# Kernel optimization log

Measured on AMD Instinct MI355X. Metric: run time of the kernel, lower is better.

Reference implementation:

```python
import jax, jax.numpy as jnp
import numpy as np

N_NODES = 100000
N_EDGES = 600000
DIMS = [128, 64, 32, 2]


def gcn_conv(x, edge_index, W, b, n_nodes):
    """PyG GCNConv (eval mode): symmetric-normalized aggregation with self-loops.
    out = D^{-1/2} (A + I) D^{-1/2} (x W) + b
    """
    h = x @ W  # [N, out] -- transform first (cheaper when out < in)
    src = jnp.concatenate([edge_index[0], jnp.arange(n_nodes)])  # add self-loops
    dst = jnp.concatenate([edge_index[1], jnp.arange(n_nodes)])
    deg = jax.ops.segment_sum(jnp.ones_like(dst, dtype=h.dtype), dst,
                              num_segments=n_nodes)  # in-degree incl. self-loop
    dinv = jax.lax.rsqrt(deg)
    norm = dinv[src] * dinv[dst]  # [E+N]
    msg = norm[:, None] * h[src]  # gather + scale
    out = jax.ops.segment_sum(msg, dst, num_segments=n_nodes)  # scatter-add
    return out + b


def setup_inputs() -> dict:
    key = jax.random.key(0)
    ks = jax.random.split(key, 8)
    x = jax.random.normal(ks[0], (N_NODES, DIMS[0]), dtype=jnp.float32)
    edge_index = jax.random.randint(ks[1], (2, N_EDGES), 0, N_NODES, dtype=jnp.int64)
    inp = {"x": x, "edge_index": edge_index}
    for i in range(3):
        fan_in, fan_out = DIMS[i], DIMS[i + 1]
        s = 1.0 / np.sqrt(fan_in)
        inp[f"W{i+1}"] = jax.random.uniform(ks[2 + 2 * i], (fan_in, fan_out),
                                            minval=-s, maxval=s, dtype=jnp.float32)
        inp[f"b{i+1}"] = jnp.zeros((fan_out,), dtype=jnp.float32)
    return inp


def reference(x, edge_index, W1, b1, W2, b2, W3, b3):
    # 3 stacked GCNConv layers with ReLU; dropout is identity in eval mode.
    n = x.shape[0]
    x = jax.nn.relu(gcn_conv(x, edge_index, W1, b1, n))
    x = jax.nn.relu(gcn_conv(x, edge_index, W2, b2, n))
    x = jax.nn.relu(gcn_conv(x, edge_index, W3, b3, n))
    return x
```

## Files before the change

### kernel.cpp

```cpp
#include <hip/hip_runtime.h>
#include <math.h>


#define FULL_GRID 2048
#define PARTS 8

typedef const __attribute__((address_space(1))) void* gas_ptr;
typedef __attribute__((address_space(3))) void* las_ptr;

__device__ __forceinline__ void gld16(const void* g, void* l) {
  __builtin_amdgcn_global_load_lds((gas_ptr)g, (las_ptr)l, 16, 0, 0);
}

__global__ __launch_bounds__(256) void k_zero(int* __restrict__ p, int n4) {
  int i = blockIdx.x * blockDim.x + threadIdx.x;
  const int stride = gridDim.x * blockDim.x;
  int4* p4 = (int4*)p;
  for (; i < n4; i += stride) p4[i] = make_int4(0, 0, 0, 0);
}

__global__ __launch_bounds__(256) void k_detect(const unsigned int* __restrict__ words,
                                                int* __restrict__ flag) {
  __shared__ int sm[256];
  int cnt = 0;
  #pragma unroll
  for (int j = 0; j < 8; ++j) {
    int idx = (threadIdx.x * 8 + j) * 2 + 1;
    cnt += (words[idx] == 0u) ? 1 : 0;
  }
  sm[threadIdx.x] = cnt;
  __syncthreads();
  for (int off = 128; off > 0; off >>= 1) {
    if (threadIdx.x < off) sm[threadIdx.x] += sm[threadIdx.x + off];
    __syncthreads();
  }
  if (threadIdx.x == 0) flag[0] = (sm[0] > 1024) ? 1 : 0;
}

__global__ __launch_bounds__(256) void k_hist(const void* __restrict__ eraw, int E,
                                              int N, const int* __restrict__ flag,
                                              int* __restrict__ counts) {
  const int is64 = flag[0];
  const int part = blockIdx.x & (PARTS - 1);
  const int lo = (int)((long long)N * part / PARTS);
  const int hi = (int)((long long)N * (part + 1) / PARTS);
  int i = (blockIdx.x >> 3) * blockDim.x + threadIdx.x;
  const int stride = (gridDim.x >> 3) * blockDim.x;
  if (is64) {
    const long long* e = (const long long*)eraw;
    for (; i < E; i += stride) {
      const int d = (int)e[(long long)E + i];
      if (d >= lo && d < hi) atomicAdd(&counts[d], 1);
    }
  } else {
    const int* e = (const int*)eraw;
    for (; i < E; i += stride) {
      const int d = e[E + i];
      if (d >= lo && d < hi) atomicAdd(&counts[d], 1);
    }
  }
}

__global__ __launch_bounds__(1024) void k_scan1(const int* __restrict__ counts,
                                                int* __restrict__ scanned,
                                                int* __restrict__ partials, int n) {
  __shared__ int sm[1024];
  const int i = blockIdx.x * 1024 + threadIdx.x;
  const int v = (i < n) ? counts[i] : 0;
  sm[threadIdx.x] = v;
  __syncthreads();
  for (int off = 1; off < 1024; off <<= 1) {
    int t = sm[threadIdx.x];
    int u = (threadIdx.x >= off) ? sm[threadIdx.x - off] : 0;
    __syncthreads();
    sm[threadIdx.x] = t + u;
    __syncthreads();
  }
  const int inc = sm[threadIdx.x];
  if (i < n) scanned[i] = inc - v;
  if (threadIdx.x == 1023) partials[blockIdx.x] = inc;
}

__global__ __launch_bounds__(1024) void k_scan2(int* __restrict__ partials, int nb) {
  __shared__ int sm[1024];
  const int v = (threadIdx.x < nb) ? partials[threadIdx.x] : 0;
  sm[threadIdx.x] = v;
  __syncthreads();
  for (int off = 1; off < 1024; off <<= 1) {
    int t = sm[threadIdx.x];
    int u = (threadIdx.x >= off) ? sm[threadIdx.x - off] : 0;
    __syncthreads();
    sm[threadIdx.x] = t + u;
    __syncthreads();
  }
  if (threadIdx.x < nb) partials[threadIdx.x] = sm[threadIdx.x] - v;
}

__global__ __launch_bounds__(256) void k_scan3(const int* __restrict__ scanned,
                                               const int* __restrict__ partials,
                                               const int* __restrict__ counts,
                                               int* __restrict__ offsets,
                                               int* __restrict__ cursor,
                                               float* __restrict__ dinv, int n) {
  int i = blockIdx.x * blockDim.x + threadIdx.x;
  const int stride = gridDim.x * blockDim.x;
  for (; i < n; i += stride) {
    const int o = scanned[i] + partials[i >> 10];
    offsets[i] = o;
    cursor[i] = o;
    dinv[i] = rsqrtf((float)counts[i] + 1.0f);
  }
}

__global__ __launch_bounds__(256) void k_fill(const void* __restrict__ eraw, int E,
                                              int N, const int* __restrict__ flag,
                                              int* __restrict__ cursor,
                                              int* __restrict__ elist) {
  const int is64 = flag[0];
  const int part = blockIdx.x & (PARTS - 1);
  const int lo = (int)((long long)N * part / PARTS);
  const int hi = (int)((long long)N * (part + 1) / PARTS);
  int i = (blockIdx.x >> 3) * blockDim.x + threadIdx.x;
  const int stride = (gridDim.x >> 3) * blockDim.x;
  if (is64) {
    const long long* e = (const long long*)eraw;
    for (; i < E; i += stride) {
      const int d = (int)e[(long long)E + i];
      if (d >= lo && d < hi) {
        const int s = (int)e[i];
        elist[atomicAdd(&cursor[d], 1)] = s;
      }
    }
  } else {
    const int* e = (const int*)eraw;
    for (; i < E; i += stride) {
      const int d = e[E + i];
      if (d >= lo && d < hi) {
        const int s = e[i];
        elist[atomicAdd(&cursor[d], 1)] = s;
      }
    }
  }
}

template <int F_IN, int F_OUT, int TILE_M, int KC, int THREADS>
__global__ __launch_bounds__(THREADS) void k_transform(const float* __restrict__ X,
                                                       const float* __restrict__ W,
                                                       const float* __restrict__ dinv,
                                                       float* __restrict__ H, int n) {
  constexpr int COLT = F_OUT / 4;
  constexpr int ROWT = THREADS / COLT;
  constexpr int TM = TILE_M / ROWT;
  constexpr int NKC = F_IN / KC;
  constexpr int K4 = F_IN / 4;
  constexpr int NWB = (NKC > 1) ? 2 : 1;
  static_assert(TM * ROWT == TILE_M && COLT * 4 == F_OUT, "tiling");
  static_assert((TILE_M * F_IN * 4) % 1024 == 0 && (KC * F_OUT * 4) % 1024 == 0, "segs");
  static_assert(K4 >= 8, "swizzle range");
  static_assert(ROWT % 8 == 0, "swizzle invariance across r");

  __shared__ __align__(16) float Xs[TILE_M * F_IN];
  __shared__ __align__(16) float Ws[NWB][KC * F_OUT];

  const int tid = threadIdx.x;
  const int lane = tid & 63;
  const int wid = tid >> 6;
  constexpr int NWAVES = THREADS / 64;
  const long long base = (long long)blockIdx.x * TILE_M;

  const float4* __restrict__ X4 = (const float4*)X;
  if (base + TILE_M <= n) {
    constexpr int SEGS = TILE_M * F_IN * 4 / 1024;
    constexpr int PW = SEGS / NWAVES;
    #pragma unroll
    for (int j = 0; j < PW; ++j) {
      const int seg = wid * PW + j;
      const int slot = seg * 64 + lane;
      const int row = slot / K4;
      const int c = slot % K4;
      const int ksrc = c ^ (row & 7);
      gld16(&X4[(base + row) * K4 + ksrc], &Xs[seg * 256]);
    }
  } else {
    for (int slot = tid; slot < TILE_M * K4; slot += THREADS) {
      const int row = slot / K4;
      const int c = slot % K4;
      float4 v = make_float4(0.f, 0.f, 0.f, 0.f);
      if (base + row < n) v = X4[(base + row) * K4 + (c ^ (row & 7))];
      ((float4*)Xs)[slot] = v;
    }
  }

  constexpr int WSEG = KC * F_OUT * 4 / 1024;
  constexpr int WPW = WSEG / NWAVES;
  static_assert(WPW >= 1, "W seg per wave");
  {
    #pragma unroll
    for (int j = 0; j < WPW; ++j) {
      const int seg = wid * WPW + j;
      gld16(W + seg * 256 + lane * 4, &Ws[0][seg * 256]);
    }
  }

  const int ct = tid % COLT;
  const int rt = tid / COLT;
  const int sw = rt & 7;

  float4 acc[TM];
  #pragma unroll
  for (int r = 0; r < TM; ++r) acc[r] = make_float4(0.f, 0.f, 0.f, 0.f);

  const float4* Xs4 = (const float4*)Xs;

  for (int kc = 0; kc < NKC; ++kc) {
    __syncthreads();
    if (NKC > 1 && kc + 1 < NKC) {
      const float* wb = W + (kc + 1) * KC * F_OUT;
      #pragma unroll
      for (int j = 0; j < WPW; ++j) {
        const int seg = wid * WPW + j;
        gld16(wb + seg * 256 + lane * 4, &Ws[(kc + 1) & (NWB - 1)][seg * 256]);
      }
    }
    const float4* Ws4 = (const float4*)Ws[kc & (NWB - 1)];
    #pragma unroll
    for (int k4 = 0; k4 < KC / 4; ++k4) {
      const int kk = kc * (KC / 4) + k4;
      float4 wv0 = Ws4[(k4 * 4 + 0) * COLT + ct];
      float4 wv1 = Ws4[(k4 * 4 + 1) * COLT + ct];
      float4 wv2 = Ws4[(k4 * 4 + 2) * COLT + ct];
      float4 wv3 = Ws4[(k4 * 4 + 3) * COLT + ct];
      #pragma unroll
      for (int r = 0; r < TM; ++r) {
        const float4 xv = Xs4[(rt + r * ROWT) * K4 + (kk ^ sw)];
        acc[r].x = fmaf(xv.x, wv0.x, acc[r].x);
        acc[r].y = fmaf(xv.x, wv0.y, acc[r].y);
        acc[r].z = fmaf(xv.x, wv0.z, acc[r].z);
        acc[r].w = fmaf(xv.x, wv0.w, acc[r].w);
        acc[r].x = fmaf(xv.y, wv1.x, acc[r].x);
        acc[r].y = fmaf(xv.y, wv1.y, acc[r].y);
        acc[r].z = fmaf(xv.y, wv1.z, acc[r].z);
        acc[r].w = fmaf(xv.y, wv1.w, acc[r].w);
        acc[r].x = fmaf(xv.z, wv2.x, acc[r].x);
        acc[r].y = fmaf(xv.z, wv2.y, acc[r].y);
        acc[r].z = fmaf(xv.z, wv2.z, acc[r].z);
        acc[r].w = fmaf(xv.z, wv2.w, acc[r].w);
        acc[r].x = fmaf(xv.w, wv3.x, acc[r].x);
        acc[r].y = fmaf(xv.w, wv3.y, acc[r].y);
        acc[r].z = fmaf(xv.w, wv3.z, acc[r].z);
        acc[r].w = fmaf(xv.w, wv3.w, acc[r].w);
      }
    }
  }

  #pragma unroll
  for (int r = 0; r < TM; ++r) {
    const long long row = base + rt + r * ROWT;
    if (row < n) {
      const float di = dinv[row];
      float4 v = acc[r];
      v.x *= di; v.y *= di; v.z *= di; v.w *= di;
      *(float4*)&H[row * F_OUT + ct * 4] = v;
    }
  }
}

template <int F, bool RELU_OUT, bool FUSE_W3>
__global__ __launch_bounds__(256) void k_aggregate(const float* __restrict__ HS,
                                                   const float* __restrict__ dinv,
                                                   const int* __restrict__ offsets,
                                                   const int* __restrict__ counts,
                                                   const int* __restrict__ elist,
                                                   const float* __restrict__ bias,
                                                   const float* __restrict__ W3,
                                                   float* __restrict__ out, int n) {
  const int f = threadIdx.x % F;
  const int grp = threadIdx.x / F;
  constexpr int GRPS = 256 / F;
  const float bf = bias[f];
  float w30 = 0.f, w31 = 0.f;
  if (FUSE_W3) { w30 = W3[f * 2 + 0]; w31 = W3[f * 2 + 1]; }

  for (long long d = (long long)blockIdx.x * GRPS + grp; d < n;
       d += (long long)gridDim.x * GRPS) {
    const float di = dinv[d];
    float acc = HS[d * F + f];
    const int start = offsets[d];
    const int cnt = counts[d];
    for (int j = 0; j < cnt; j += 8) {
      int idx[8];
      float v[8];
      #pragma unroll
      for (int t = 0; t < 8; ++t) {
        const int jj = (j + t < cnt) ? (j + t) : j;
        idx[t] = elist[start + jj];
      }
      #pragma unroll
      for (int t = 0; t < 8; ++t) v[t] = HS[(long long)idx[t] * F + f];
      #pragma unroll
      for (int t = 0; t < 8; ++t) acc += (j + t < cnt) ? v[t] : 0.f;
    }

    float r = fmaf(di, acc, bf);
    if (RELU_OUT) r = fmaxf(r, 0.f);
    if (!FUSE_W3) {
      out[d * F + f] = r;
    } else {
      float t0 = r * w30, t1 = r * w31;
      #pragma unroll
      for (int m = 1; m < 32; m <<= 1) {
        t0 += __shfl_xor(t0, m, 64);
        t1 += __shfl_xor(t1, m, 64);
      }
      if (f == 0) {
        out[d * 2 + 0] = di * t0;
        out[d * 2 + 1] = di * t1;
      }
    }
  }
}

extern "C" void kernel_launch(void* const* d_in, const int* in_sizes, int n_in,
                              void* d_out, int out_size, void* d_ws, size_t ws_size,
                              hipStream_t stream) {
  const float* x = (const float*)d_in[0];
  const void* eraw = d_in[1];
  const float* W1 = (const float*)d_in[2];
  const float* b1 = (const float*)d_in[3];
  const float* W2 = (const float*)d_in[4];
  const float* b2 = (const float*)d_in[5];
  const float* W3 = (const float*)d_in[6];
  const float* b3 = (const float*)d_in[7];
  float* out = (float*)d_out;

  const int N = in_sizes[0] / 128;
  const int E = in_sizes[1] / 2;

  char* ws = (char*)d_ws;
  size_t off = 0;
  auto alloc = [&](size_t bytes) -> char* {
    char* p = ws + off;
    off = (off + bytes + 255) & ~(size_t)255;
    return p;
  };
  int*   flag     = (int*)alloc(256);
  int*   counts   = (int*)alloc((size_t)N * 4 + 16);
  int*   scanned  = (int*)alloc((size_t)N * 4);
  int*   partials = (int*)alloc(1024 * 4);
  int*   offsets  = (int*)alloc((size_t)N * 4);
  int*   cursor   = (int*)alloc((size_t)N * 4);
  int*   elist    = (int*)alloc((size_t)E * 4);
  float* dinv     = (float*)alloc((size_t)N * 4);
  float* hbuf     = (float*)alloc((size_t)N * 64 * 4);
  float* obuf     = (float*)alloc((size_t)N * 64 * 4);
  float* h2buf    = (float*)alloc((size_t)N * 32 * 4);
  (void)ws_size; (void)n_in; (void)out_size;

  k_zero<<<128, 256, 0, stream>>>(counts, (N + 3) / 4);
  k_detect<<<1, 256, 0, stream>>>((const unsigned int*)eraw, flag);
  k_hist<<<FULL_GRID, 256, 0, stream>>>(eraw, E, N, flag, counts);
  const int NB = (N + 1023) >> 10;
  k_scan1<<<NB, 1024, 0, stream>>>(counts, scanned, partials, N);
  k_scan2<<<1, 1024, 0, stream>>>(partials, NB);
  k_scan3<<<(N + 255) / 256, 256, 0, stream>>>(scanned, partials, counts, offsets,
                                               cursor, dinv, N);
  k_fill<<<FULL_GRID, 256, 0, stream>>>(eraw, E, N, flag, cursor, elist);

  k_transform<128, 64, 128, 16, 256><<<(N + 127) / 128, 256, 0, stream>>>(
      x, W1, dinv, hbuf, N);
  k_aggregate<64, true, false><<<(N + 3) / 4, 256, 0, stream>>>(
      hbuf, dinv, offsets, counts, elist, b1, nullptr, obuf, N);

  k_transform<64, 32, 128, 64, 256><<<(N + 127) / 128, 256, 0, stream>>>(
      obuf, W2, dinv, h2buf, N);
  k_aggregate<32, true, true><<<(N + 7) / 8, 256, 0, stream>>>(
      h2buf, dinv, offsets, counts, elist, b2, W3, hbuf, N);

  k_aggregate<2, true, false><<<(N + 127) / 128, 256, 0, stream>>>(
      hbuf, dinv, offsets, counts, elist, b3, nullptr, out, N);
}
```

Measured before the change: 197.1 us.

## Make transform kernel persistent with resident W and double-buffered X tiles

After: 190.7 us. -3.2%, faster.

```diff
diff --git a/kernel.cpp b/kernel.cpp
--- a/kernel.cpp
+++ b/kernel.cpp
@@ -143,96 +143,91 @@
   }
 }
 
-template <int F_IN, int F_OUT, int TILE_M, int KC, int THREADS>
+template <int F_IN, int F_OUT, int TILE_M, int THREADS>
 __global__ __launch_bounds__(THREADS) void k_transform(const float* __restrict__ X,
                                                        const float* __restrict__ W,
                                                        const float* __restrict__ dinv,
-                                                       float* __restrict__ H, int n) {
+                                                       float* __restrict__ H, int n,
+                                                       int ntiles) {
   constexpr int COLT = F_OUT / 4;
   constexpr int ROWT = THREADS / COLT;
   constexpr int TM = TILE_M / ROWT;
-  constexpr int NKC = F_IN / KC;
   constexpr int K4 = F_IN / 4;
-  constexpr int NWB = (NKC > 1) ? 2 : 1;
+  constexpr int NWAVES = THREADS / 64;
+  constexpr int XSEG = TILE_M * F_IN * 4 / 1024;
+  constexpr int XPW = XSEG / NWAVES;
+  constexpr int WSEG = F_IN * F_OUT * 4 / 1024;
+  constexpr int WPW = (WSEG + NWAVES - 1) / NWAVES;
   static_assert(TM * ROWT == TILE_M && COLT * 4 == F_OUT, "tiling");
-  static_assert((TILE_M * F_IN * 4) % 1024 == 0 && (KC * F_OUT * 4) % 1024 == 0, "segs");
+  static_assert(XPW * NWAVES == XSEG, "X segs per wave");
   static_assert(K4 >= 8, "swizzle range");
   static_assert(ROWT % 8 == 0, "swizzle invariance across r");
 
-  __shared__ __align__(16) float Xs[TILE_M * F_IN];
-  __shared__ __align__(16) float Ws[NWB][KC * F_OUT];
+  __shared__ __align__(16) float Xs[2][TILE_M * F_IN];
+  __shared__ __align__(16) float Ws[F_IN * F_OUT];
 
   const int tid = threadIdx.x;
   const int lane = tid & 63;
   const int wid = tid >> 6;
-  constexpr int NWAVES = THREADS / 64;
-  const long long base = (long long)blockIdx.x * TILE_M;
-
   const float4* __restrict__ X4 = (const float4*)X;
-  if (base + TILE_M <= n) {
-    constexpr int SEGS = TILE_M * F_IN * 4 / 1024;
-    constexpr int PW = SEGS / NWAVES;
-    #pragma unroll
-    for (int j = 0; j < PW; ++j) {
-      const int seg = wid * PW + j;
-      const int slot = seg * 64 + lane;
-      const int row = slot / K4;
-      const int c = slot % K4;
-      const int ksrc = c ^ (row & 7);
-      gld16(&X4[(base + row) * K4 + ksrc], &Xs[seg * 256]);
-    }
-  } else {
-    for (int slot = tid; slot < TILE_M * K4; slot += THREADS) {
-      const int row = slot / K4;
-      const int c = slot % K4;
-      float4 v = make_float4(0.f, 0.f, 0.f, 0.f);
-      if (base + row < n) v = X4[(base + row) * K4 + (c ^ (row & 7))];
-      ((float4*)Xs)[slot] = v;
-    }
-  }
-
-  constexpr int WSEG = KC * F_OUT * 4 / 1024;
-  constexpr int WPW = WSEG / NWAVES;
-  static_assert(WPW >= 1, "W seg per wave");
-  {
-    #pragma unroll
-    for (int j = 0; j < WPW; ++j) {
-      const int seg = wid * WPW + j;
-      gld16(W + seg * 256 + lane * 4, &Ws[0][seg * 256]);
-    }
-  }
+
+  #pragma unroll
+  for (int j = 0; j < WPW; ++j) {
+    const int seg = wid * WPW + j;
+    if (seg < WSEG) gld16(W + seg * 256 + lane * 4, &Ws[seg * 256]);
+  }
+
+  auto stage = [&](int buf, int tile) {
+    const long long base = (long long)tile * TILE_M;
+    if (base + TILE_M <= n) {
+      #pragma unroll
+      for (int j = 0; j < XPW; ++j) {
+        const int seg = wid * XPW + j;
+        const int slot = seg * 64 + lane;
+        const int row = slot / K4;
+        const int c = slot % K4;
+        gld16(&X4[(base + row) * K4 + (c ^ (row & 7))], &Xs[buf][seg * 256]);
+      }
+    } else {
+      for (int slot = tid; slot < TILE_M * K4; slot += THREADS) {
+        const int row = slot / K4;
+        const int c = slot % K4;
+        float4 v = make_float4(0.f, 0.f, 0.f, 0.f);
+        if (base + row < n) v = X4[(base + row) * K4 + (c ^ (row & 7))];
+        ((float4*)Xs[buf])[slot] = v;
+      }
+    }
+  };
 
   const int ct = tid % COLT;
   const int rt = tid / COLT;
   const int sw = rt & 7;
-
-  float4 acc[TM];
-  #pragma unroll
-  for (int r = 0; r < TM; ++r) acc[r] = make_float4(0.f, 0.f, 0.f, 0.f);
-
-  const float4* Xs4 = (const float4*)Xs;
-
-  for (int kc = 0; kc < NKC; ++kc) {
-    __syncthreads();
-    if (NKC > 1 && kc + 1 < NKC) {
-      const float* wb = W + (kc + 1) * KC * F_OUT;
-      #pragma unroll
-      for (int j = 0; j < WPW; ++j) {
-        const int seg = wid * WPW + j;
-        gld16(wb + seg * 256 + lane * 4, &Ws[(kc + 1) & (NWB - 1)][seg * 256]);
-      }
-    }
-    const float4* Ws4 = (const float4*)Ws[kc & (NWB - 1)];
+  const float4* Ws4 = (const float4*)Ws;
+
+  int tile = blockIdx.x;
+  if (tile < ntiles) stage(0, tile);
+  int buf = 0;
+
+  for (; tile < ntiles; tile += gridDim.x) {
+    __syncthreads();
+    const int nxt = tile + gridDim.x;
+    if (nxt < ntiles) stage(buf ^ 1, nxt);
+
+    const long long base = (long long)tile * TILE_M;
+    float4 acc[TM];
     #pragma unroll
-    for (int k4 = 0; k4 < KC / 4; ++k4) {
-      const int kk = kc * (KC / 4) + k4;
-      float4 wv0 = Ws4[(k4 * 4 + 0) * COLT + ct];
-      float4 wv1 = Ws4[(k4 * 4 + 1) * COLT + ct];
-      float4 wv2 = Ws4[(k4 * 4 + 2) * COLT + ct];
-      float4 wv3 = Ws4[(k4 * 4 + 3) * COLT + ct];
+    for (int r = 0; r < TM; ++r) acc[r] = make_float4(0.f, 0.f, 0.f, 0.f);
+    const float4* Xs4 = (const float4*)Xs[buf];
+
+    #pragma unroll 4
+    for (int k4 = 0; k4 < K4; ++k4) {
+      const float4 wv0 = Ws4[(k4 * 4 + 0) * COLT + ct];
+      const float4 wv1 = Ws4[(k4 * 4 + 1) * COLT + ct];
+      const float4 wv2 = Ws4[(k4 * 4 + 2) * COLT + ct];
+      const float4 wv3 = Ws4[(k4 * 4 + 3) * COLT + ct];
       #pragma unroll
       for (int r = 0; r < TM; ++r) {
-        const float4 xv = Xs4[(rt + r * ROWT) * K4 + (kk ^ sw)];
+        const float4 xv = Xs4[(rt + r * ROWT) * K4 + (k4 ^ sw)];
         acc[r].x = fmaf(xv.x, wv0.x, acc[r].x);
         acc[r].y = fmaf(xv.x, wv0.y, acc[r].y);
         acc[r].z = fmaf(xv.x, wv0.z, acc[r].z);
@@ -251,17 +246,19 @@
         acc[r].w = fmaf(xv.w, wv3.w, acc[r].w);
       }
     }
-  }
-
-  #pragma unroll
-  for (int r = 0; r < TM; ++r) {
-    const long long row = base + rt + r * ROWT;
-    if (row < n) {
-      const float di = dinv[row];
-      float4 v = acc[r];
-      v.x *= di; v.y *= di; v.z *= di; v.w *= di;
-      *(float4*)&H[row * F_OUT + ct * 4] = v;
-    }
+
+    #pragma unroll
+    for (int r = 0; r < TM; ++r) {
+      const long long row = base + rt + r * ROWT;
+      if (row < n) {
+        const float di = dinv[row];
+        float4 v = acc[r];
+        v.x *= di; v.y *= di; v.z *= di; v.w *= di;
+        *(float4*)&H[row * F_OUT + ct * 4] = v;
+      }
+    }
+    __syncthreads();
+    buf ^= 1;
   }
 }
 
@@ -366,13 +363,19 @@
                                                cursor, dinv, N);
   k_fill<<<FULL_GRID, 256, 0, stream>>>(eraw, E, N, flag, cursor, elist);
 
-  k_transform<128, 64, 128, 16, 256><<<(N + 127) / 128, 256, 0, stream>>>(
-      x, W1, dinv, hbuf, N);
+  {
+    const int ntiles = (N + 95) / 96;
+    k_transform<128, 64, 96, 512><<<256, 512, 0, stream>>>(x, W1, dinv, hbuf, N,
+                                                           ntiles);
+  }
   k_aggregate<64, true, false><<<(N + 3) / 4, 256, 0, stream>>>(
       hbuf, dinv, offsets, counts, elist, b1, nullptr, obuf, N);
 
-  k_transform<64, 32, 128, 64, 256><<<(N + 127) / 128, 256, 0, stream>>>(
-      obuf, W2, dinv, h2buf, N);
+  {
+    const int ntiles = (N + 127) / 128;
+    k_transform<64, 32, 128, 512><<<512, 512, 0, stream>>>(obuf, W2, dinv, h2buf, N,
+                                                           ntiles);
+  }
   k_aggregate<32, true, true><<<(N + 7) / 8, 256, 0, stream>>>(
       h2buf, dinv, offsets, counts, elist, b2, W3, hbuf, N);
 
```

## Replace LDS-tiled transform GEMM with register-blocked per-lane row kernel

Applied to the files above, without the earlier changes.

Result: slower. 242.3 us (+23.0%).

```diff
diff --git a/kernel.cpp b/kernel.cpp
--- a/kernel.cpp
+++ b/kernel.cpp
@@ -4,13 +4,6 @@
 
 #define FULL_GRID 2048
 #define PARTS 8
-
-typedef const __attribute__((address_space(1))) void* gas_ptr;
-typedef __attribute__((address_space(3))) void* las_ptr;
-
-__device__ __forceinline__ void gld16(const void* g, void* l) {
-  __builtin_amdgcn_global_load_lds((gas_ptr)g, (las_ptr)l, 16, 0, 0);
-}
 
 __global__ __launch_bounds__(256) void k_zero(int* __restrict__ p, int n4) {
   int i = blockIdx.x * blockDim.x + threadIdx.x;
@@ -143,124 +136,87 @@
   }
 }
 
-template <int F_IN, int F_OUT, int TILE_M, int KC, int THREADS>
-__global__ __launch_bounds__(THREADS) void k_transform(const float* __restrict__ X,
-                                                       const float* __restrict__ W,
-                                                       const float* __restrict__ dinv,
-                                                       float* __restrict__ H, int n) {
-  constexpr int COLT = F_OUT / 4;
-  constexpr int ROWT = THREADS / COLT;
-  constexpr int TM = TILE_M / ROWT;
-  constexpr int NKC = F_IN / KC;
+__device__ __forceinline__ float f4get(const float4& v, int j) {
+  return j == 0 ? v.x : (j == 1 ? v.y : (j == 2 ? v.z : v.w));
+}
+
+template <int F_IN, int F_OUT, int TM, int TN>
+__global__ __launch_bounds__((F_OUT / TN) * 64) void k_transform_reg(
+    const float* __restrict__ X, const float* __restrict__ W,
+    const float* __restrict__ dinv, float* __restrict__ H, int n) {
   constexpr int K4 = F_IN / 4;
-  constexpr int NWB = (NKC > 1) ? 2 : 1;
-  static_assert(TM * ROWT == TILE_M && COLT * 4 == F_OUT, "tiling");
-  static_assert((TILE_M * F_IN * 4) % 1024 == 0 && (KC * F_OUT * 4) % 1024 == 0, "segs");
-  static_assert(K4 >= 8, "swizzle range");
-  static_assert(ROWT % 8 == 0, "swizzle invariance across r");
-
-  __shared__ __align__(16) float Xs[TILE_M * F_IN];
-  __shared__ __align__(16) float Ws[NWB][KC * F_OUT];
-
-  const int tid = threadIdx.x;
-  const int lane = tid & 63;
-  const int wid = tid >> 6;
-  constexpr int NWAVES = THREADS / 64;
-  const long long base = (long long)blockIdx.x * TILE_M;
-
+  constexpr int TN4 = TN / 4;
+  constexpr int ROWS = TM * 64;
+
+  const int lane = threadIdx.x & 63;
+  const int cg = __builtin_amdgcn_readfirstlane(threadIdx.x >> 6);
+  const long long base = (long long)blockIdx.x * ROWS;
   const float4* __restrict__ X4 = (const float4*)X;
-  if (base + TILE_M <= n) {
-    constexpr int SEGS = TILE_M * F_IN * 4 / 1024;
-    constexpr int PW = SEGS / NWAVES;
+  const float* __restrict__ Wc = W + cg * TN;
+
+  long long row[TM];
+  bool ok[TM];
+  #pragma unroll
+  for (int g = 0; g < TM; ++g) {
+    row[g] = base + g * 64 + lane;
+    ok[g] = row[g] < n;
+  }
+
+  float4 acc[TM][TN4];
+  #pragma unroll
+  for (int g = 0; g < TM; ++g)
     #pragma unroll
-    for (int j = 0; j < PW; ++j) {
-      const int seg = wid * PW + j;
-      const int slot = seg * 64 + lane;
-      const int row = slot / K4;
-      const int c = slot % K4;
-      const int ksrc = c ^ (row & 7);
-      gld16(&X4[(base + row) * K4 + ksrc], &Xs[seg * 256]);
-    }
-  } else {
-    for (int slot = tid; slot < TILE_M * K4; slot += THREADS) {
-      const int row = slot / K4;
-      const int c = slot % K4;
-      float4 v = make_float4(0.f, 0.f, 0.f, 0.f);
-      if (base + row < n) v = X4[(base + row) * K4 + (c ^ (row & 7))];
-      ((float4*)Xs)[slot] = v;
-    }
-  }
-
-  constexpr int WSEG = KC * F_OUT * 4 / 1024;
-  constexpr int WPW = WSEG / NWAVES;
-  static_assert(WPW >= 1, "W seg per wave");
-  {
+    for (int c = 0; c < TN4; ++c) acc[g][c] = make_float4(0.f, 0.f, 0.f, 0.f);
+
+  float4 xcur[TM];
+  #pragma unroll
+  for (int g = 0; g < TM; ++g)
+    xcur[g] = ok[g] ? X4[row[g] * K4] : make_float4(0.f, 0.f, 0.f, 0.f);
+
+  #pragma unroll 4
+  for (int k4 = 0; k4 < K4; ++k4) {
+    float4 xnxt[TM];
+    if (k4 + 1 < K4) {
+      #pragma unroll
+      for (int g = 0; g < TM; ++g)
+        xnxt[g] = ok[g] ? X4[row[g] * K4 + k4 + 1] : make_float4(0.f, 0.f, 0.f, 0.f);
+    }
+    float w[4][TN];
     #pragma unroll
-    for (int j = 0; j < WPW; ++j) {
-      const int seg = wid * WPW + j;
-      gld16(W + seg * 256 + lane * 4, &Ws[0][seg * 256]);
-    }
-  }
-
-  const int ct = tid % COLT;
-  const int rt = tid / COLT;
-  const int sw = rt & 7;
-
-  float4 acc[TM];
-  #pragma unroll
-  for (int r = 0; r < TM; ++r) acc[r] = make_float4(0.f, 0.f, 0.f, 0.f);
-
-  const float4* Xs4 = (const float4*)Xs;
-
-  for (int kc = 0; kc < NKC; ++kc) {
-    __syncthreads();
-    if (NKC > 1 && kc + 1 < NKC) {
-      const float* wb = W + (kc + 1) * KC * F_OUT;
-      #pragma unroll
-      for (int j = 0; j < WPW; ++j) {
-        const int seg = wid * WPW + j;
-        gld16(wb + seg * 256 + lane * 4, &Ws[(kc + 1) & (NWB - 1)][seg * 256]);
-      }
-    }
-    const float4* Ws4 = (const float4*)Ws[kc & (NWB - 1)];
+    for (int kk = 0; kk < 4; ++kk)
+      #pragma unroll
+      for (int c = 0; c < TN; ++c) w[kk][c] = Wc[(k4 * 4 + kk) * F_OUT + c];
+
     #pragma unroll
-    for (int k4 = 0; k4 < KC / 4; ++k4) {
-      const int kk = kc * (KC / 4) + k4;
-      float4 wv0 = Ws4[(k4 * 4 + 0) * COLT + ct];
-      float4 wv1 = Ws4[(k4 * 4 + 1) * COLT + ct];
-      float4 wv2 = Ws4[(k4 * 4 + 2) * COLT + ct];
-      float4 wv3 = Ws4[(k4 * 4 + 3) * COLT + ct];
-      #pragma unroll
-      for (int r = 0; r < TM; ++r) {
-        const float4 xv = Xs4[(rt + r * ROWT) * K4 + (kk ^ sw)];
-        acc[r].x = fmaf(xv.x, wv0.x, acc[r].x);
-        acc[r].y = fmaf(xv.x, wv0.y, acc[r].y);
-        acc[r].z = fmaf(xv.x, wv0.z, acc[r].z);
-        acc[r].w = fmaf(xv.x, wv0.w, acc[r].w);
-        acc[r].x = fmaf(xv.y, wv1.x, acc[r].x);
-        acc[r].y = fmaf(xv.y, wv1.y, acc[r].y);
-        acc[r].z = fmaf(xv.y, wv1.z, acc[r].z);
-        acc[r].w = fmaf(xv.y, wv1.w, acc[r].w);
-        acc[r].x = fmaf(xv.z, wv2.x, acc[r].x);
-        acc[r].y = fmaf(xv.z, wv2.y, acc[r].y);
-        acc[r].z = fmaf(xv.z, wv2.z, acc[r].z);
-        acc[r].w = fmaf(xv.z, wv2.w, acc[r].w);
-        acc[r].x = fmaf(xv.w, wv3.x, acc[r].x);
-        acc[r].y = fmaf(xv.w, wv3.y, acc[r].y);
-        acc[r].z = fmaf(xv.w, wv3.z, acc[r].z);
-        acc[r].w = fmaf(xv.w, wv3.w, acc[r].w);
-      }
-    }
-  }
-
-  #pragma unroll
-  for (int r = 0; r < TM; ++r) {
-    const long long row = base + rt + r * ROWT;
-    if (row < n) {
-      const float di = dinv[row];
-      float4 v = acc[r];
-      v.x *= di; v.y *= di; v.z *= di; v.w *= di;
-      *(float4*)&H[row * F_OUT + ct * 4] = v;
+    for (int g = 0; g < TM; ++g) {
+      #pragma unroll
+      for (int kk = 0; kk < 4; ++kk) {
+        const float xs = f4get(xcur[g], kk);
+        #pragma unroll
+        for (int c = 0; c < TN4; ++c) {
+          acc[g][c].x = fmaf(xs, w[kk][c * 4 + 0], acc[g][c].x);
+          acc[g][c].y = fmaf(xs, w[kk][c * 4 + 1], acc[g][c].y);
+          acc[g][c].z = fmaf(xs, w[kk][c * 4 + 2], acc[g][c].z);
+          acc[g][c].w = fmaf(xs, w[kk][c * 4 + 3], acc[g][c].w);
+        }
+      }
+    }
+    if (k4 + 1 < K4) {
+      #pragma unroll
+      for (int g = 0; g < TM; ++g) xcur[g] = xnxt[g];
+    }
+  }
+
+  #pragma unroll
+  for (int g = 0; g < TM; ++g) {
+    if (ok[g]) {
+      const float di = dinv[row[g]];
+      #pragma unroll
+      for (int c = 0; c < TN4; ++c) {
+        float4 v = acc[g][c];
+        v.x *= di; v.y *= di; v.z *= di; v.w *= di;
+        *(float4*)&H[row[g] * F_OUT + cg * TN + c * 4] = v;
+      }
     }
   }
 }
@@ -366,12 +322,12 @@
                                                cursor, dinv, N);
   k_fill<<<FULL_GRID, 256, 0, stream>>>(eraw, E, N, flag, cursor, elist);
 
-  k_transform<128, 64, 128, 16, 256><<<(N + 127) / 128, 256, 0, stream>>>(
+  k_transform_reg<128, 64, 4, 8><<<(N + 255) / 256, 512, 0, stream>>>(
       x, W1, dinv, hbuf, N);
   k_aggregate<64, true, false><<<(N + 3) / 4, 256, 0, stream>>>(
       hbuf, dinv, offsets, counts, elist, b1, nullptr, obuf, N);
 
-  k_transform<64, 32, 128, 64, 256><<<(N + 127) / 128, 256, 0, stream>>>(
+  k_transform_reg<64, 32, 4, 8><<<(N + 255) / 256, 256, 0, stream>>>(
       obuf, W2, dinv, h2buf, N);
   k_aggregate<32, true, true><<<(N + 7) / 8, 256, 0, stream>>>(
       h2buf, dinv, offsets, counts, elist, b2, W3, hbuf, N);
```
